# Kernel optimization log

Measured on AMD Instinct MI355X. Metric: run time of the kernel, lower is better.

## Reference

```python
import jax, jax.numpy as jnp
import numpy as np

B, S, H, L = 64, 512, 1024, 9  # batch, seq_len, hidden_size, num_labels


def setup_inputs() -> dict:
    key = jax.random.key(0)
    ks = jax.random.split(key, 8)
    hidden = jax.random.normal(ks[0], (B, S, H), dtype=jnp.float32)
    W = jax.random.normal(ks[1], (L, H), dtype=jnp.float32) * 0.02
    b = jnp.zeros((L,), dtype=jnp.float32)
    # pytorch-crf initializes transitions uniform in [-0.1, 0.1]
    start_transitions = jax.random.uniform(ks[2], (L,), jnp.float32, -0.1, 0.1)
    end_transitions = jax.random.uniform(ks[3], (L,), jnp.float32, -0.1, 0.1)
    transitions = jax.random.uniform(ks[4], (L, L), jnp.float32, -0.1, 0.1)
    labels = jax.random.randint(ks[5], (B, S), 0, L)
    # variable lengths; first timestep always valid (required by pytorch-crf)
    lengths = jax.random.randint(ks[6], (B,), S // 4, S + 1)
    mask = (jnp.arange(S)[None, :] < lengths[:, None]).astype(jnp.int32)
    return {
        "hidden": hidden, "W": W, "b": b,
        "start_transitions": start_transitions,
        "end_transitions": end_transitions,
        "transitions": transitions,
        "labels": labels, "mask": mask,
    }


def reference(hidden, W, b, start_transitions, end_transitions, transitions, labels, mask):
    # classifier: emissions [B,S,L] (fp32, matching .float() cast in the module)
    emissions = jnp.einsum("bsh,lh->bsl", hidden, W) + b
    maskf = mask.astype(emissions.dtype)

    # ---- numerator: score of the gold path ----
    emit = jnp.take_along_axis(emissions, labels[..., None], axis=-1)[..., 0]  # [B,S]
    trans_sc = transitions[labels[:, :-1], labels[:, 1:]]                       # [B,S-1]
    score = (start_transitions[labels[:, 0]]
             + jnp.sum(emit * maskf, axis=1)
             + jnp.sum(trans_sc * maskf[:, 1:], axis=1))
    seq_ends = jnp.sum(mask, axis=1) - 1                     # last valid index per example
    last_tags = labels[jnp.arange(labels.shape[0]), seq_ends]
    score = score + end_transitions[last_tags]

    # ---- denominator: log partition via masked forward recurrence ----
    alpha0 = start_transitions[None, :] + emissions[:, 0]    # [B,L]
    em_t = jnp.swapaxes(emissions, 0, 1)[1:]                 # [S-1,B,L]
    mk_t = jnp.swapaxes(mask, 0, 1)[1:].astype(bool)         # [S-1,B]

    def step(alpha, xs):
        e_t, m_t = xs
        # broadcast: alpha[b,i] + transitions[i,j] + e_t[b,j]
        nxt = jax.scipy.special.logsumexp(
            alpha[:, :, None] + transitions[None, :, :] + e_t[:, None, :], axis=1)
        alpha = jnp.where(m_t[:, None], nxt, alpha)
        return alpha, None

    alpha, _ = jax.lax.scan(step, alpha0, (em_t, mk_t))
    logZ = jax.scipy.special.logsumexp(alpha + end_transitions[None, :], axis=1)  # [B]

    llh = score - logZ
    loss = -jnp.mean(llh)  # reduction='mean', negated in the module
    return loss
```

## Files before the change

kernel.cpp:

```cpp
#include <hip/hip_runtime.h>
#include <hip/hip_bf16.h>

#define LOG2E 1.4426950408889634f
#define LN2   0.6931471805599453f

constexpr int Bn = 64, Sn = 512, Hn = 1024, Ln = 9;
constexpr int CL = 24;
constexpr int NC = 22;

typedef __attribute__((ext_vector_type(8))) short short8v;
typedef __attribute__((ext_vector_type(4))) float f32x4;

__device__ __forceinline__ float fexp2(float x) { return __builtin_amdgcn_exp2f(x); }
__device__ __forceinline__ float flog2(float x) { return __builtin_amdgcn_logf(x); }
__device__ __forceinline__ unsigned cvtpk(float lo, float hi) {
    unsigned r; asm("v_cvt_pk_bf16_f32 %0, %1, %2" : "=v"(r) : "v"(lo), "v"(hi)); return r;
}
__device__ __forceinline__ float max9(const float* s) {
    return fmaxf(fmaxf(fmaxf(s[0], s[1]), fmaxf(s[2], s[3])),
                 fmaxf(fmaxf(s[4], s[5]), fmaxf(s[6], fmaxf(s[7], s[8]))));
}

__global__ __launch_bounds__(256) void emis_kernel(
    const float* __restrict__ hidden, const float* __restrict__ W,
    const float* __restrict__ bias, float* __restrict__ emis,
    float* __restrict__ out0)
{
    __shared__ __align__(16) unsigned short wfrag[32][64][8];
    const int tid = threadIdx.x, lane = tid & 63, w = tid >> 6;

    if (blockIdx.x == 0 && tid == 0) out0[0] = 0.f;

    for (int f = tid; f < 32 * 64; f += 256) {
        const int s = f >> 6, l = f & 63;
        const int j = l & 15, k0 = s * 32 + ((l >> 4) << 3);
        uint4 pk = {0u, 0u, 0u, 0u};
        if (j < Ln) {
            float4 a = *(const float4*)(W + j * Hn + k0);
            float4 c = *(const float4*)(W + j * Hn + k0 + 4);
            pk.x = cvtpk(a.x, a.y); pk.y = cvtpk(a.z, a.w);
            pk.z = cvtpk(c.x, c.y); pk.w = cvtpk(c.z, c.w);
        }
        *(uint4*)&wfrag[s][l][0] = pk;
    }
    __syncthreads();

    const int row0 = blockIdx.x * 64 + w * 16;
    const float* hptr = hidden + (size_t)(row0 + (lane & 15)) * Hn + ((lane >> 4) << 3);

    f32x4 acc = {0.f, 0.f, 0.f, 0.f};
    #pragma unroll 4
    for (int s = 0; s < 32; ++s) {
        float4 a0 = *(const float4*)(hptr + s * 32);
        float4 a1 = *(const float4*)(hptr + s * 32 + 4);
        uint4 ap;
        ap.x = cvtpk(a0.x, a0.y); ap.y = cvtpk(a0.z, a0.w);
        ap.z = cvtpk(a1.x, a1.y); ap.w = cvtpk(a1.z, a1.w);
        short8v Av = *(short8v*)&ap;
        short8v Bv = *(const short8v*)&wfrag[s][lane][0];
        acc = __builtin_amdgcn_mfma_f32_16x16x32_bf16(Av, Bv, acc, 0, 0, 0);
    }

    const int col = lane & 15;
    if (col < Ln) {
        const float bv = bias[col];
        #pragma unroll
        for (int r = 0; r < 4; ++r) {
            const int row = ((lane >> 4) << 2) + r;
            emis[(size_t)(row0 + row) * Ln + col] = acc[r] + bv;
        }
    }
}

__global__ __launch_bounds__(256, 1) void crf_kernel(
    const float* __restrict__ emis, const float* __restrict__ st,
    const float* __restrict__ et,   const float* __restrict__ T,
    const int* __restrict__ labels, const int* __restrict__ mask,
    float* __restrict__ out)
{
    __shared__ __align__(16) float e_lds[Sn * Ln];
    __shared__ float M_lds[NC][Ln][10];
    __shared__ float part[4];
    __shared__ int   sl_sh;

    const int b    = blockIdx.x;
    const int tid  = threadIdx.x;
    const int w    = tid >> 6;
    const int lane = tid & 63;

    {
        const float4* src = (const float4*)(emis + (size_t)b * Sn * Ln);
        float4* dst = (float4*)e_lds;
        for (int i = tid; i < (Sn * Ln) / 4; i += 256) dst[i] = src[i];
    }
    float E[Ln][Ln];
    #pragma unroll
    for (int k = 0; k < Ln; ++k)
        #pragma unroll
        for (int j = 0; j < Ln; ++j)
            E[k][j] = fexp2(T[k * Ln + j] * LOG2E);
    if (w == 3) {
        const int* mb = mask + b * Sn;
        int s = 0;
        #pragma unroll
        for (int r = 0; r < Sn / 64; ++r) s += mb[lane + r * 64];
        #pragma unroll
        for (int off = 32; off; off >>= 1) s += __shfl_xor(s, off);
        if (lane == 0) sl_sh = s;
    }
    __syncthreads();

    const int sl    = sl_sh;
    const int nreal = (sl - 1 + CL - 1) / CL;

    {
        const int ul = lane / 9;
        const int i  = lane - ul * 9;
        const int c  = w * 7 + ul;
        const int t0 = 1 + c * CL;
        if (ul < 7 && c < nreal) {
            const int nst = min(CL, sl - t0);
            float u[Ln];
            {
                const float* e0 = e_lds + t0 * Ln;
                #pragma unroll
                for (int j = 0; j < Ln; ++j)
                    u[j] = E[i][j] * fexp2(fmaf(e0[j], LOG2E, -4.f));
            }
            float extra = 0.f;
            for (int s = 1; s < nst; ++s) {
                const float* es = e_lds + (t0 + s) * Ln;
                float q[Ln];
                #pragma unroll
                for (int j = 0; j < Ln; ++j)
                    q[j] = fexp2(fmaf(es[j], LOG2E, -4.f));
                float v[Ln];
                #pragma unroll
                for (int j = 0; j < Ln; ++j) v[j] = 0.f;
                #pragma unroll
                for (int kk = 0; kk < Ln; ++kk) {
                    const float uk = u[kk];
                    #pragma unroll
                    for (int j = 0; j < Ln; ++j)
                        v[j] = fmaf(uk, E[kk][j], v[j]);
                }
                #pragma unroll
                for (int j = 0; j < Ln; ++j) u[j] = v[j] * q[j];
                if (s == 12) {
                    float m  = max9(u);
                    float iv = 1.f / m;
                    #pragma unroll
                    for (int j = 0; j < Ln; ++j) u[j] *= iv;
                    extra = flog2(m);
                }
            }
            #pragma unroll
            for (int j = 0; j < Ln; ++j)
                M_lds[c][i][j] = flog2(u[j]) + extra + 4.f * (float)nst;
        }
    }
    __syncthreads();

    float logZ = 0.f;
    if (w == 0) {
        const int j9 = lane < Ln ? lane : Ln - 1;
        float al[Ln];
        #pragma unroll
        for (int j = 0; j < Ln; ++j) al[j] = (st[j] + e_lds[j]) * LOG2E;
        for (int c = 0; c < nreal; ++c) {
            float s[Ln];
            #pragma unroll
            for (int k = 0; k < Ln; ++k) s[k] = al[k] + M_lds[c][k][j9];
            float p = max9(s);
            float sum = fexp2(s[0] - p);
            #pragma unroll
            for (int k = 1; k < Ln; ++k) sum += fexp2(s[k] - p);
            float aj = p + flog2(sum);
            #pragma unroll
            for (int k = 0; k < Ln; ++k) al[k] = __shfl(aj, k);
        }
        float z[Ln];
        #pragma unroll
        for (int j = 0; j < Ln; ++j) z[j] = al[j] + et[j] * LOG2E;
        float p = max9(z);
        float sum = fexp2(z[0] - p);
        #pragma unroll
        for (int j = 1; j < Ln; ++j) sum += fexp2(z[j] - p);
        logZ = (p + flog2(sum)) * LN2;
    } else {
        const int* lb = labels + b * Sn;
        float sc = 0.f;
        for (int t = (w - 1) * 64 + lane; t < sl; t += 192) {
            int lt = lb[t];
            sc += e_lds[t * Ln + lt];
            if (t >= 1) sc += T[lb[t - 1] * Ln + lt];
        }
        #pragma unroll
        for (int off = 32; off; off >>= 1) sc += __shfl_xor(sc, off);
        if (w == 1 && lane == 0) sc += st[lb[0]] + et[lb[sl - 1]];
        if (lane == 0) part[w - 1] = sc;
    }
    __syncthreads();

    if (w == 0 && lane == 0) {
        float llh = part[0] + part[1] + part[2] - logZ;
        atomicAdd(out, llh * (-1.f / 64.f));
    }
}

extern "C" void kernel_launch(void* const* d_in, const int* in_sizes, int n_in,
                              void* d_out, int out_size, void* d_ws, size_t ws_size,
                              hipStream_t stream) {
    const float* hidden = (const float*)d_in[0];
    const float* W      = (const float*)d_in[1];
    const float* bias   = (const float*)d_in[2];
    const float* st     = (const float*)d_in[3];
    const float* et     = (const float*)d_in[4];
    const float* T      = (const float*)d_in[5];
    const int*   labels = (const int*)d_in[6];
    const int*   mask   = (const int*)d_in[7];

    float* emis = (float*)d_ws;
    float* outp = (float*)d_out;

    emis_kernel<<<512, 256, 0, stream>>>(hidden, W, bias, emis, outp);
    crf_kernel<<<Bn, 256, 0, stream>>>(emis, st, et, T, labels, mask, outp);
}
```

Baseline: 44.88 us.

## Stage hidden rows through double-buffered LDS with coalesced loads in emission GEMM

The emission kernel now loads hidden rows with fully coalesced 16-byte accesses (two rows of 512 bytes per wavefront), converts them to bf16, and stages them in a double-buffered LDS tile. The next 128-column chunk is prefetched into registers while MFMAs consume the current one. The first chunk's load is issued before the W fragment setup so the two overlap. The goal is higher HBM efficiency and latency hiding on the dominant 256MB hidden read, at the cost of extra LDS traffic and a barrier per chunk.

```diff
diff --git a/kernel.cpp b/kernel.cpp
--- a/kernel.cpp
+++ b/kernel.cpp
@@ -27,9 +27,20 @@
     float* __restrict__ out0)
 {
     __shared__ __align__(16) unsigned short wfrag[32][64][8];
+    __shared__ __align__(16) unsigned short hbuf[2][4][16][136];
+
     const int tid = threadIdx.x, lane = tid & 63, w = tid >> 6;
-
     if (blockIdx.x == 0 && tid == 0) out0[0] = 0.f;
+
+    const int row0 = blockIdx.x * 64 + w * 16;
+    const char* hbase = (const char*)(hidden + (size_t)row0 * Hn);
+    const int srow = lane >> 5;
+    const int sbyt = (lane & 31) * 16;
+
+    f32x4 Lv[8];
+    #pragma unroll
+    for (int i = 0; i < 8; ++i)
+        Lv[i] = *(const f32x4*)(hbase + (size_t)(i * 2 + srow) * 4096 + sbyt);
 
     for (int f = tid; f < 32 * 64; f += 256) {
         const int s = f >> 6, l = f & 63;
@@ -43,30 +54,48 @@
         }
         *(uint4*)&wfrag[s][l][0] = pk;
     }
-    __syncthreads();
-
-    const int row0 = blockIdx.x * 64 + w * 16;
-    const float* hptr = hidden + (size_t)(row0 + (lane & 15)) * Hn + ((lane >> 4) << 3);
-
+
+    #pragma unroll
+    for (int i = 0; i < 8; ++i) {
+        uint2 pk = { cvtpk(Lv[i][0], Lv[i][1]), cvtpk(Lv[i][2], Lv[i][3]) };
+        *(uint2*)&hbuf[0][w][i * 2 + srow][(lane & 31) * 4] = pk;
+    }
+    __syncthreads();
+
+    const int r16 = lane & 15, g16 = lane >> 4;
     f32x4 acc = {0.f, 0.f, 0.f, 0.f};
-    #pragma unroll 4
-    for (int s = 0; s < 32; ++s) {
-        float4 a0 = *(const float4*)(hptr + s * 32);
-        float4 a1 = *(const float4*)(hptr + s * 32 + 4);
-        uint4 ap;
-        ap.x = cvtpk(a0.x, a0.y); ap.y = cvtpk(a0.z, a0.w);
-        ap.z = cvtpk(a1.x, a1.y); ap.w = cvtpk(a1.z, a1.w);
-        short8v Av = *(short8v*)&ap;
-        short8v Bv = *(const short8v*)&wfrag[s][lane][0];
-        acc = __builtin_amdgcn_mfma_f32_16x16x32_bf16(Av, Bv, acc, 0, 0, 0);
-    }
-
-    const int col = lane & 15;
+
+    #pragma unroll
+    for (int p = 0; p < 8; ++p) {
+        const int cur = p & 1;
+        if (p < 7) {
+            #pragma unroll
+            for (int i = 0; i < 8; ++i)
+                Lv[i] = *(const f32x4*)(hbase + (size_t)(i * 2 + srow) * 4096
+                                               + (p + 1) * 512 + sbyt);
+        }
+        #pragma unroll
+        for (int s = 0; s < 4; ++s) {
+            short8v Av = *(const short8v*)&hbuf[cur][w][r16][s * 32 + g16 * 8];
+            short8v Bv = *(const short8v*)&wfrag[p * 4 + s][lane][0];
+            acc = __builtin_amdgcn_mfma_f32_16x16x32_bf16(Av, Bv, acc, 0, 0, 0);
+        }
+        if (p < 7) {
+            #pragma unroll
+            for (int i = 0; i < 8; ++i) {
+                uint2 pk = { cvtpk(Lv[i][0], Lv[i][1]), cvtpk(Lv[i][2], Lv[i][3]) };
+                *(uint2*)&hbuf[cur ^ 1][w][i * 2 + srow][(lane & 31) * 4] = pk;
+            }
+            __syncthreads();
+        }
+    }
+
+    const int col = r16;
     if (col < Ln) {
         const float bv = bias[col];
         #pragma unroll
         for (int r = 0; r < 4; ++r) {
-            const int row = ((lane >> 4) << 2) + r;
+            const int row = (g16 << 2) + r;
             emis[(size_t)(row0 + row) * Ln + col] = acc[r] + bv;
         }
     }
```

After: 44.26 us. No clear change (-1.4%).
